# Optimization experiments

Measured on AMD Instinct MI355X. Metric: run time of the kernel, lower is better.

Reference implementation:

```python
import jax, jax.numpy as jnp
import numpy as np

B, LQ, LK, D, H = 8, 512, 512, 512, 128

def setup_inputs() -> dict:
    key = jax.random.key(0)
    k1, k2, k3, k4, k5 = jax.random.split(key, 5)
    qs = jax.random.normal(k1, (B, LQ, D), dtype=jnp.float32)
    ks = jax.random.normal(k2, (B, LK, D), dtype=jnp.float32)
    # Dense kernels: flax Dense stores kernel as [in_features, out_features]
    Wq = jax.random.normal(k3, (D, H), dtype=jnp.float32) / np.sqrt(D)
    Wk = jax.random.normal(k4, (D, H), dtype=jnp.float32) / np.sqrt(D)
    wv = jax.random.normal(k5, (H,), dtype=jnp.float32) / np.sqrt(H)
    return {"qs": qs, "ks": ks, "Wq": Wq, "Wk": Wk, "wv": wv}

def reference(qs, ks, Wq, Wk, wv):
    # Project queries and keys into the shared hidden space: [B,Lq,H], [B,Lk,H]
    q = jnp.einsum("bqd,dh->bqh", qs, Wq)
    k = jnp.einsum("bkd,dh->bkh", ks, Wk)
    # Broadcast-add -> tanh -> linear reduce over H: scores [B,Lq,Lk]
    feats = jnp.tanh(q[:, :, None, :] + k[:, None, :, :])  # [B,Lq,Lk,H]
    return jnp.einsum("bqkh,h->bqk", feats, wv)
```

## Files before the change

kernel.cpp:

```cpp
#include <hip/hip_runtime.h>
#include <hip/hip_bf16.h>
#include <cstdint>

#define B_   8
#define LQ_  512
#define LK_  512
#define D_   512
#define H_   128

typedef __attribute__((ext_vector_type(8))) short  short8;
typedef __attribute__((ext_vector_type(4))) float  float4v;

#define TANH_C 2.8853900817779268f

__device__ __forceinline__ short bf16rne(float x) {
  uint32_t u = __float_as_uint(x);
  return (short)((u + 0x7fffu + ((u >> 16) & 1u)) >> 16);
}

__global__ __launch_bounds__(256) void prep_kernel(
    const float* __restrict__ Wq, const float* __restrict__ Wk,
    const float* __restrict__ wv,
    short* __restrict__ WqF, short* __restrict__ WkF,
    float* __restrict__ w2, float* __restrict__ W0buf) {
  int g = blockIdx.x * 256 + threadIdx.x;
  if (blockIdx.x == 0) {
    int t = threadIdx.x;
    if (t < H_) w2[t] = -2.0f * wv[t];
    if (t == H_) {
      float s = 0.f;
      for (int h = 0; h < H_; ++h) s += wv[h];
      W0buf[0] = s;
    }
  }
  int m = g >> 13;
  int r = g & 8191;
  int l  = r & 63;
  int kb = (r >> 6) & 15;
  int nt = r >> 10;
  int col = nt * 16 + (l & 15);
  int k0  = kb * 32 + ((l >> 4) << 3);
  const float* W = m ? Wk : Wq;
  short8 f;
#pragma unroll
  for (int j = 0; j < 8; ++j) f[j] = bf16rne(W[(k0 + j) * H_ + col]);
  ((short8*)(m ? WkF : WqF))[r] = f;
}

__global__ __launch_bounds__(256) void proj_kernel(
    const float* __restrict__ qs, const float* __restrict__ ks,
    const short* __restrict__ WqF, const short* __restrict__ WkF,
    float* __restrict__ qp, float* __restrict__ kp) {
  int blk  = blockIdx.x;
  int wave = threadIdx.x >> 6;
  int l    = threadIdx.x & 63;
  int rt   = blk >> 1;
  int ct   = (blk & 1) * 4 + wave;
  int grow = rt * 16;
  int m    = (grow >= 4096) ? 1 : 0;
  int r0   = grow - (m ? 4096 : 0);
  const float*  A  = m ? ks : qs;
  const short8* BF = (const short8*)(m ? WkF : WqF);
  float* out = m ? kp : qp;

  float4v acc = (float4v){0.f, 0.f, 0.f, 0.f};

  int quad = l >> 4;
  int arow = r0 + (l & 15);
  const float* aptr = A + (size_t)arow * D_ + quad * 8;

#pragma unroll 4
  for (int kb = 0; kb < 16; ++kb) {
    float4v a0 = *(const float4v*)(aptr + kb * 32);
    float4v a1 = *(const float4v*)(aptr + kb * 32 + 4);
    short8 af;
#pragma unroll
    for (int j = 0; j < 4; ++j) { af[j] = bf16rne(a0[j]); af[j + 4] = bf16rne(a1[j]); }
    short8 bf = BF[(ct * 16 + kb) * 64 + l];
    acc = __builtin_amdgcn_mfma_f32_16x16x32_bf16(af, bf, acc, 0, 0, 0);
  }

#pragma unroll
  for (int r = 0; r < 4; ++r) {
    int row = r0 + quad * 4 + r;
    int col = ct * 16 + (l & 15);
    out[(size_t)row * H_ + col] = __builtin_amdgcn_exp2f(acc[r] * TANH_C);
  }
}

__global__ __launch_bounds__(256) void score_kernel(
    const float* __restrict__ qp, const float* __restrict__ kp,
    const float* __restrict__ w2, const float* __restrict__ W0buf,
    float* __restrict__ out) {
  __shared__ float qt[64 * 68];
  __shared__ float kt[64 * 68];
  __shared__ float wl[H_];

  int b = blockIdx.z, qtile = blockIdx.y, ktile = blockIdx.x;
  int t = threadIdx.x;
  int tx = t & 15, ty = t >> 4;

  const float* qbase = qp + (size_t)(b * LQ_ + qtile * 64) * H_;
  const float* kbase = kp + (size_t)(b * LK_ + ktile * 64) * H_;

  float W0 = W0buf[0];

  if (t < 32) *(float4v*)&wl[t * 4] = *(const float4v*)&w2[t * 4];

  float accs[4][4];
  const float4v ones = (float4v){1.f, 1.f, 1.f, 1.f};
#pragma unroll
  for (int i = 0; i < 4; ++i)
#pragma unroll
    for (int j = 0; j < 4; ++j) accs[i][j] = 0.f;

  int lr = t >> 4, lc = t & 15;

  for (int hc = 0; hc < 2; ++hc) {
    __syncthreads();
#pragma unroll
    for (int s = 0; s < 4; ++s) {
      int row = lr + 16 * s;
      *(float4v*)&qt[row * 68 + lc * 4] =
          *(const float4v*)&qbase[row * H_ + hc * 64 + lc * 4];
      *(float4v*)&kt[row * 68 + lc * 4] =
          *(const float4v*)&kbase[row * H_ + hc * 64 + lc * 4];
    }
    __syncthreads();

#pragma unroll 2
    for (int h0 = 0; h0 < 64; h0 += 4) {
      float4v qv[4], kv[4];
#pragma unroll
      for (int i = 0; i < 4; ++i)
        qv[i] = *(const float4v*)&qt[(ty + 16 * i) * 68 + h0];
#pragma unroll
      for (int j = 0; j < 4; ++j)
        kv[j] = *(const float4v*)&kt[(tx + 16 * j) * 68 + h0];
      float4v w4 = *(const float4v*)&wl[hc * 64 + h0];

#pragma unroll
      for (int i = 0; i < 4; ++i)
#pragma unroll
        for (int j = 0; j < 4; ++j) {
          float4v den = __builtin_elementwise_fma(qv[i], kv[j], ones);
          float d01 = den[0] * den[1];
          float d23 = den[2] * den[3];
          float n01 = fmaf(w4[1], den[0], w4[0] * den[1]);
          float n23 = fmaf(w4[3], den[2], w4[2] * den[3]);
          float big = fmaf(n01, d23, n23 * d01);
          float r   = __builtin_amdgcn_rcpf(d01 * d23);
          accs[i][j] = fmaf(big, r, accs[i][j]);
        }
    }
  }

  size_t ob = (size_t)(b * LQ_ + qtile * 64) * LK_ + ktile * 64;
#pragma unroll
  for (int i = 0; i < 4; ++i)
#pragma unroll
    for (int j = 0; j < 4; ++j)
      out[ob + (size_t)(ty + 16 * i) * LK_ + tx + 16 * j] = W0 + accs[i][j];
}

extern "C" void kernel_launch(void* const* d_in, const int* in_sizes, int n_in,
                              void* d_out, int out_size, void* d_ws, size_t ws_size,
                              hipStream_t stream) {
  const float* qs = (const float*)d_in[0];
  const float* ks = (const float*)d_in[1];
  const float* Wq = (const float*)d_in[2];
  const float* Wk = (const float*)d_in[3];
  const float* wv = (const float*)d_in[4];
  float* out = (float*)d_out;

  char* ws = (char*)d_ws;
  short* WqF  = (short*)ws;
  short* WkF  = (short*)(ws + (128 << 10));
  float* qp   = (float*)(ws + (256 << 10));
  float* kp   = (float*)(ws + (256 << 10) + (2 << 20));
  float* w2   = (float*)(ws + (256 << 10) + (4 << 20));
  float* W0b  = (float*)(ws + (256 << 10) + (4 << 20) + 512);

  prep_kernel<<<64, 256, 0, stream>>>(Wq, Wk, wv, WqF, WkF, w2, W0b);
  proj_kernel<<<1024, 256, 0, stream>>>(qs, ks, WqF, WkF, qp, kp);
  score_kernel<<<dim3(8, 8, 8), 256, 0, stream>>>(qp, kp, w2, W0b, out);
}
```

Baseline: 116.5 us.

## Split hidden dim across two thread halves in score kernel, widen proj tiles

The score kernel now runs 512 threads per block. Each half handles one 64-wide chunk of the hidden dimension, with the full 128-wide q/k tiles loaded into shared memory once. The two partial sums are combined through shared memory before the store. The projection kernel has each wave compute two column tiles so the A operand is reused, which halves the grid. The aim is more resident waves to hide latency and fewer tile reloads and barriers, at the cost of more shared memory per block and an extra reduction step.

```diff
diff --git a/kernel.cpp b/kernel.cpp
--- a/kernel.cpp
+++ b/kernel.cpp
@@ -54,20 +54,21 @@
   int blk  = blockIdx.x;
   int wave = threadIdx.x >> 6;
   int l    = threadIdx.x & 63;
-  int rt   = blk >> 1;
-  int ct   = (blk & 1) * 4 + wave;
-  int grow = rt * 16;
+  int grow = blk * 16;
   int m    = (grow >= 4096) ? 1 : 0;
   int r0   = grow - (m ? 4096 : 0);
   const float*  A  = m ? ks : qs;
   const short8* BF = (const short8*)(m ? WkF : WqF);
   float* out = m ? kp : qp;
 
-  float4v acc = (float4v){0.f, 0.f, 0.f, 0.f};
+  float4v acc[2];
+  acc[0] = (float4v){0.f, 0.f, 0.f, 0.f};
+  acc[1] = (float4v){0.f, 0.f, 0.f, 0.f};
 
   int quad = l >> 4;
   int arow = r0 + (l & 15);
   const float* aptr = A + (size_t)arow * D_ + quad * 8;
+  int t0 = wave * 2;
 
 #pragma unroll 4
   for (int kb = 0; kb < 16; ++kb) {
@@ -76,29 +77,35 @@
     short8 af;
 #pragma unroll
     for (int j = 0; j < 4; ++j) { af[j] = bf16rne(a0[j]); af[j + 4] = bf16rne(a1[j]); }
-    short8 bf = BF[(ct * 16 + kb) * 64 + l];
-    acc = __builtin_amdgcn_mfma_f32_16x16x32_bf16(af, bf, acc, 0, 0, 0);
-  }
-
-#pragma unroll
-  for (int r = 0; r < 4; ++r) {
-    int row = r0 + quad * 4 + r;
-    int col = ct * 16 + (l & 15);
-    out[(size_t)row * H_ + col] = __builtin_amdgcn_exp2f(acc[r] * TANH_C);
-  }
-}
-
-__global__ __launch_bounds__(256) void score_kernel(
+#pragma unroll
+    for (int tt = 0; tt < 2; ++tt) {
+      short8 bf = BF[((t0 + tt) * 16 + kb) * 64 + l];
+      acc[tt] = __builtin_amdgcn_mfma_f32_16x16x32_bf16(af, bf, acc[tt], 0, 0, 0);
+    }
+  }
+
+#pragma unroll
+  for (int tt = 0; tt < 2; ++tt)
+#pragma unroll
+    for (int r = 0; r < 4; ++r) {
+      int row = r0 + quad * 4 + r;
+      int col = (t0 + tt) * 16 + (l & 15);
+      out[(size_t)row * H_ + col] = __builtin_amdgcn_exp2f(acc[tt][r] * TANH_C);
+    }
+}
+
+__global__ __launch_bounds__(512, 4) void score_kernel(
     const float* __restrict__ qp, const float* __restrict__ kp,
     const float* __restrict__ w2, const float* __restrict__ W0buf,
     float* __restrict__ out) {
-  __shared__ float qt[64 * 68];
-  __shared__ float kt[64 * 68];
+  __shared__ __align__(16) float qt[64 * 132];
+  __shared__ __align__(16) float kt[64 * 132];
   __shared__ float wl[H_];
 
   int b = blockIdx.z, qtile = blockIdx.y, ktile = blockIdx.x;
   int t = threadIdx.x;
-  int tx = t & 15, ty = t >> 4;
+  int tx = t & 15, ty = (t >> 4) & 15;
+  int hc = t >> 8;
 
   const float* qbase = qp + (size_t)(b * LQ_ + qtile * 64) * H_;
   const float* kbase = kp + (size_t)(b * LK_ + ktile * 64) * H_;
@@ -107,6 +114,19 @@
 
   if (t < 32) *(float4v*)&wl[t * 4] = *(const float4v*)&w2[t * 4];
 
+  {
+    int lrow = t >> 3, lc = t & 7;
+#pragma unroll
+    for (int s = 0; s < 4; ++s) {
+      int h4 = lc + 8 * s;
+      *(float4v*)&qt[lrow * 132 + h4 * 4] =
+          *(const float4v*)&qbase[lrow * H_ + h4 * 4];
+      *(float4v*)&kt[lrow * 132 + h4 * 4] =
+          *(const float4v*)&kbase[lrow * H_ + h4 * 4];
+    }
+  }
+  __syncthreads();
+
   float accs[4][4];
   const float4v ones = (float4v){1.f, 1.f, 1.f, 1.f};
 #pragma unroll
@@ -114,53 +134,53 @@
 #pragma unroll
     for (int j = 0; j < 4; ++j) accs[i][j] = 0.f;
 
-  int lr = t >> 4, lc = t & 15;
-
-  for (int hc = 0; hc < 2; ++hc) {
-    __syncthreads();
-#pragma unroll
-    for (int s = 0; s < 4; ++s) {
-      int row = lr + 16 * s;
-      *(float4v*)&qt[row * 68 + lc * 4] =
-          *(const float4v*)&qbase[row * H_ + hc * 64 + lc * 4];
-      *(float4v*)&kt[row * 68 + lc * 4] =
-          *(const float4v*)&kbase[row * H_ + hc * 64 + lc * 4];
-    }
-    __syncthreads();
-
-#pragma unroll 2
-    for (int h0 = 0; h0 < 64; h0 += 4) {
-      float4v qv[4], kv[4];
-#pragma unroll
-      for (int i = 0; i < 4; ++i)
-        qv[i] = *(const float4v*)&qt[(ty + 16 * i) * 68 + h0];
+  int hb = hc * 64;
+#pragma unroll 1
+  for (int h0 = 0; h0 < 64; h0 += 4) {
+    float4v qv[4], kv[4];
+#pragma unroll
+    for (int i = 0; i < 4; ++i)
+      qv[i] = *(const float4v*)&qt[(ty + 16 * i) * 132 + hb + h0];
+#pragma unroll
+    for (int j = 0; j < 4; ++j)
+      kv[j] = *(const float4v*)&kt[(tx + 16 * j) * 132 + hb + h0];
+    float4v w4 = *(const float4v*)&wl[hb + h0];
+
+#pragma unroll
+    for (int i = 0; i < 4; ++i)
+#pragma unroll
+      for (int j = 0; j < 4; ++j) {
+        float4v den = __builtin_elementwise_fma(qv[i], kv[j], ones);
+        float d01 = den[0] * den[1];
+        float d23 = den[2] * den[3];
+        float n01 = fmaf(w4[1], den[0], w4[0] * den[1]);
+        float n23 = fmaf(w4[3], den[2], w4[2] * den[3]);
+        float big = fmaf(n01, d23, n23 * d01);
+        float r   = __builtin_amdgcn_rcpf(d01 * d23);
+        accs[i][j] = fmaf(big, r, accs[i][j]);
+      }
+  }
+
+  __syncthreads();
+  if (t >= 256) {
+    int p = t - 256;
+#pragma unroll
+    for (int i = 0; i < 4; ++i)
+      *(float4v*)&qt[p * 16 + i * 4] =
+          (float4v){accs[i][0], accs[i][1], accs[i][2], accs[i][3]};
+  }
+  __syncthreads();
+  if (t < 256) {
+    size_t ob = (size_t)(b * LQ_ + qtile * 64) * LK_ + ktile * 64;
+#pragma unroll
+    for (int i = 0; i < 4; ++i) {
+      float4v p = *(const float4v*)&qt[t * 16 + i * 4];
 #pragma unroll
       for (int j = 0; j < 4; ++j)
-        kv[j] = *(const float4v*)&kt[(tx + 16 * j) * 68 + h0];
-      float4v w4 = *(const float4v*)&wl[hc * 64 + h0];
-
-#pragma unroll
-      for (int i = 0; i < 4; ++i)
-#pragma unroll
-        for (int j = 0; j < 4; ++j) {
-          float4v den = __builtin_elementwise_fma(qv[i], kv[j], ones);
-          float d01 = den[0] * den[1];
-          float d23 = den[2] * den[3];
-          float n01 = fmaf(w4[1], den[0], w4[0] * den[1]);
-          float n23 = fmaf(w4[3], den[2], w4[2] * den[3]);
-          float big = fmaf(n01, d23, n23 * d01);
-          float r   = __builtin_amdgcn_rcpf(d01 * d23);
-          accs[i][j] = fmaf(big, r, accs[i][j]);
-        }
-    }
-  }
-
-  size_t ob = (size_t)(b * LQ_ + qtile * 64) * LK_ + ktile * 64;
-#pragma unroll
-  for (int i = 0; i < 4; ++i)
-#pragma unroll
-    for (int j = 0; j < 4; ++j)
-      out[ob + (size_t)(ty + 16 * i) * LK_ + tx + 16 * j] = W0 + accs[i][j];
+        out[ob + (size_t)(ty + 16 * i) * LK_ + tx + 16 * j] =
+            W0 + accs[i][j] + p[j];
+    }
+  }
 }
 
 extern "C" void kernel_launch(void* const* d_in, const int* in_sizes, int n_in,
@@ -182,6 +202,6 @@
   float* W0b  = (float*)(ws + (256 << 10) + (4 << 20) + 512);
 
   prep_kernel<<<64, 256, 0, stream>>>(Wq, Wk, wv, WqF, WkF, w2, W0b);
-  proj_kernel<<<1024, 256, 0, stream>>>(qs, ks, WqF, WkF, qp, kp);
-  score_kernel<<<dim3(8, 8, 8), 256, 0, stream>>>(qp, kp, w2, W0b, out);
-}
+  proj_kernel<<<512, 256, 0, stream>>>(qs, ks, WqF, WkF, qp, kp);
+  score_kernel<<<dim3(8, 8, 8), 512, 0, stream>>>(qp, kp, w2, W0b, out);
+}
```

New measurement: 109.4 us. -6.0%, faster.
